# Kernel tuning notes

Measured on AMD Instinct MI355X. Metric: run time of the kernel, lower is better.

The kernel has to match this reference:

```python
import jax, jax.numpy as jnp
import numpy as np
from jax import lax

T, Nn, K, IN, H1, H2, G, P, HEADS = 64, 2048, 32, 256, 128, 128, 256, 60, 3


def setup_inputs() -> dict:
    key = jax.random.key(0)
    ks = jax.random.split(key, 20)
    s = 0.05  # weight scale to keep activations sane
    return {
        'h': jax.random.normal(ks[0], (T, Nn, IN), jnp.float32),
        'neigh': jax.random.randint(ks[1], (Nn, K), 0, Nn),
        'Npop': jnp.ones((1,), jnp.float32) * 1e6,
        'I': jax.random.uniform(ks[2], (T,), jnp.float32) * 1e4,
        'R': jax.random.uniform(ks[3], (T,), jnp.float32) * 1e4,
        'S': jax.random.uniform(ks[4], (T,), jnp.float32) * 9e5,
        'It': jax.random.uniform(ks[5], (T,), jnp.float32),
        'Rt': jax.random.uniform(ks[6], (T,), jnp.float32),
        'fc1': jax.random.normal(ks[7], (HEADS, IN, H1), jnp.float32) * s,
        'fc2': jax.random.normal(ks[8], (HEADS * H1, H2), jnp.float32) * s,
        'gru_Wih': jax.random.normal(ks[9], (3 * G, H2), jnp.float32) * s,
        'gru_Whh': jax.random.normal(ks[10], (3 * G, G), jnp.float32) * s,
        'gru_bih': jax.random.normal(ks[11], (3 * G,), jnp.float32) * s,
        'gru_bhh': jax.random.normal(ks[12], (3 * G,), jnp.float32) * s,
        'res1_W': jax.random.normal(ks[13], (2 * P, G + 2), jnp.float32) * s,
        'res1_b': jax.random.normal(ks[14], (2 * P,), jnp.float32) * s,
        'res2_W': jax.random.normal(ks[15], (2, G + 2), jnp.float32) * s,
        'res2_b': jax.random.normal(ks[16], (2,), jnp.float32) * s,
        'hx0': jax.random.normal(ks[17], (G,), jnp.float32),
    }


def _input_attention(iz, neigh):
    # cosine^4 edge scores, unnormalized weighted sum of neighbor feats
    src = iz[neigh]                                  # [N,K,d]
    dot = jnp.einsum('nkd,nd->nk', src, iz)
    nsrc = jnp.sqrt(jnp.einsum('nkd,nkd->nk', src, src))
    ndst = jnp.sqrt(jnp.sum(iz * iz, axis=-1))[:, None]
    e = (dot / nsrc / ndst) ** 4                     # [N,K]
    return jnp.einsum('nk,nkd->nd', e, src)


def _gat_head(x, W, neigh):
    # dot-product edge attention + per-node softmax + weighted reduce
    z = x @ W                                        # [N,H]
    src = z[neigh]                                   # [N,K,H]
    e = jnp.einsum('nkd,nd->nk', src, z)             # [N,K]
    a = jax.nn.softmax(e, axis=1)
    return jnp.einsum('nk,nkd->nd', a, src)


def _gru_cell(x, hx, Wih, Whh, bih, bhh):
    gi = Wih @ x + bih                               # [3G]
    gh = Whh @ hx + bhh
    ir, iz, inn = jnp.split(gi, 3)
    hr, hz, hn = jnp.split(gh, 3)
    r = jax.nn.sigmoid(ir + hr)
    zg = jax.nn.sigmoid(iz + hz)
    n = jnp.tanh(inn + r * hn)
    return (1.0 - zg) * n + zg * hx


def reference(h, neigh, Npop, I, R, S, It, Rt, fc1, fc2, gru_Wih, gru_Whh,
              gru_bih, gru_bhh, res1_W, res1_b, res2_W, res2_b, hx0):
    Np = Npop[0]

    def step(hx, xs):
        h_t, I_t, R_t, S_t, It_t, Rt_t = xs
        ih = _input_attention(h_t, neigh)                       # [N,in]
        heads = jax.vmap(lambda W: _gat_head(ih, W, neigh))(fc1)  # [3,N,H1]
        c = jax.nn.relu(jnp.transpose(heads, (1, 0, 2)).reshape(Nn, HEADS * H1))
        c = _gat_head(c, fc2, neigh)                            # [N,H2]
        pooled = jnp.max(jax.nn.relu(c), axis=0)                # [H2]
        hx = _gru_cell(pooled, hx, gru_Wih, gru_Whh, gru_bih, gru_bhh)
        nhx = jnp.concatenate([hx, It_t[None], Rt_t[None]])     # [G+2]
        pred = res1_W @ nhx + res1_b                            # [2P]
        ab = res2_W @ nhx + res2_b
        a_s = jax.nn.sigmoid(ab[0])
        b_s = jax.nn.sigmoid(ab[1])
        new_I = pred[0::2]
        new_R = pred[1::2]

        def sir(st, _):
            lI, lR, lS = st
            dI = a_s * lI * (lS / Np) - b_s * lI
            dR = b_s * lI
            nI = lI + lax.stop_gradient(dI)
            nR = lR + lax.stop_gradient(dR)
            nS = Np - nI - nR
            return (nI, nR, nS), (dI, dR)

        _, (pI, pR) = lax.scan(sir, (I_t, R_t, S_t), None, length=P)
        return hx, (new_I, new_R, pI, pR)

    _, (new_I, new_R, phy_I, phy_R) = lax.scan(step, hx0, (h, I, R, S, It, Rt))
    return (new_I, new_R, phy_I.reshape(-1), phy_R.reshape(-1))
```

## Files before the change

### kernel.cpp

```cpp
#include <hip/hip_runtime.h>
#include <hip/hip_bf16.h>
#include <math.h>

#define T_STEPS 64
#define NN      2048
#define KN      32
#define IND     256
#define H1D     128
#define C1D     384
#define H2D     128
#define GD      256
#define PD      60
#define GRU_NB  8

typedef __attribute__((ext_vector_type(8))) short bf16x8v;
typedef __attribute__((ext_vector_type(4))) float f32x4v;

#define BITREV5_INIT {0,16,8,24,4,20,12,28,2,18,10,26,6,22,14,30, \
                      1,17,9,25,5,21,13,29,3,19,11,27,7,23,15,31}

__device__ __forceinline__ float bcast_lane(float v, int lane_imm) {
    return __uint_as_float(__builtin_amdgcn_readlane(__float_as_uint(v), lane_imm));
}

__device__ __forceinline__ void bf16_split(float v, __hip_bfloat16* hi, __hip_bfloat16* lo) {
    __hip_bfloat16 h = __float2bfloat16(v);
    *hi = h;
    *lo = __float2bfloat16(v - __bfloat162float(h));
}

__device__ __forceinline__ float xpose_reduce16(float part[16], int lane) {
#pragma unroll
    for (int i = 0; i < 8; ++i) {
        float send = (lane & 2) ? part[i] : part[i + 8];
        float keep = (lane & 2) ? part[i + 8] : part[i];
        part[i] = keep + __shfl_xor(send, 2);
    }
#pragma unroll
    for (int i = 0; i < 4; ++i) {
        float send = (lane & 4) ? part[i] : part[i + 4];
        float keep = (lane & 4) ? part[i + 4] : part[i];
        part[i] = keep + __shfl_xor(send, 4);
    }
#pragma unroll
    for (int i = 0; i < 2; ++i) {
        float send = (lane & 8) ? part[i] : part[i + 2];
        float keep = (lane & 8) ? part[i + 2] : part[i];
        part[i] = keep + __shfl_xor(send, 8);
    }
    {
        float send = (lane & 16) ? part[0] : part[1];
        float keep = (lane & 16) ? part[1] : part[0];
        part[0] = keep + __shfl_xor(send, 16);
    }
    return part[0] + __shfl_xor(part[0], 32);
}

__global__ __launch_bounds__(256) void norms_kernel(const float* __restrict__ h,
                                                    float* __restrict__ norms,
                                                    int t_base) {
    int gw   = (int)((blockIdx.x * blockDim.x + threadIdx.x) >> 6);
    int lane = threadIdx.x & 63;
    int n    = gw & (NN - 1);
    int tloc = gw >> 11;
    const float4* row = (const float4*)(h + ((size_t)(t_base + tloc) * NN + n) * IND);
    float4 v = row[lane];
    float s = v.x * v.x + v.y * v.y + v.z * v.z + v.w * v.w;
#pragma unroll
    for (int off = 32; off > 0; off >>= 1) s += __shfl_xor(s, off);
    if (lane == 0) norms[(size_t)tloc * NN + n] = sqrtf(s);
}

__global__ __launch_bounds__(256, 4) void input_attn_kernel(const float* __restrict__ h,
                                                            const int* __restrict__ neigh,
                                                            const float* __restrict__ norms,
                                                            __hip_bfloat16* __restrict__ ihHi,
                                                            __hip_bfloat16* __restrict__ ihLo,
                                                            int t_base) {
    const int BR[32] = BITREV5_INIT;
    __shared__ float hd_s[2][2][32];
    int wave    = threadIdx.x >> 6;
    int nodeloc = wave >> 1;
    int half    = wave & 1;
    int lane    = threadIdx.x & 63;
    int gw   = (int)((blockIdx.x << 1) | nodeloc);
    int n    = gw & (NN - 1);
    int tloc = gw >> 11;
    const float* hT  = h + (size_t)(t_base + tloc) * NN * IND;
    const float* nrm = norms + (size_t)tloc * NN;

    const float* dst = hT + (size_t)n * IND + half * 128;
    float d0 = dst[lane], d1 = dst[lane + 64];

    int   jreg = neigh[n * KN + (lane & 31)];
    float nj   = nrm[jreg];
    float ndst = nrm[n];

    float r0[32], r1[32], comb[16];
#pragma unroll
    for (int i = 0; i < 16; ++i) {
        int sja = __builtin_amdgcn_readlane(jreg, BR[i]);
        int sjb = __builtin_amdgcn_readlane(jreg, BR[i + 16]);
        const float* sa = hT + (size_t)sja * IND + half * 128;
        const float* sb = hT + (size_t)sjb * IND + half * 128;
        r0[i]      = sa[lane]; r1[i]      = sa[lane + 64];
        r0[i + 16] = sb[lane]; r1[i + 16] = sb[lane + 64];
        float pa = r0[i] * d0 + r1[i] * d1;
        float pb = r0[i + 16] * d0 + r1[i + 16] * d1;
        float send = (lane & 1) ? pa : pb;
        float keep = (lane & 1) ? pb : pa;
        comb[i] = keep + __shfl_xor(send, 1);
    }
#pragma unroll
    for (int i = 0; i < 32; ++i) asm volatile("" : "+v"(r0[i]), "+v"(r1[i]));
    float hdot = xpose_reduce16(comb, lane);
    if (lane < 32) hd_s[nodeloc][half][lane] = hdot;
    __syncthreads();
    float dot = hdot + hd_s[nodeloc][half ^ 1][lane & 31];

    float r  = dot / (nj * ndst);
    float r2 = r * r;
    float e  = r2 * r2;

    float a0 = 0.f, a1 = 0.f;
#pragma unroll
    for (int i = 0; i < 32; ++i) {
        float ek = bcast_lane(e, BR[i]);
        a0 += ek * r0[i];
        a1 += ek * r1[i];
    }
    size_t base = (size_t)gw * IND + half * 128;
    __hip_bfloat16 hi, lo;
    bf16_split(a0, &hi, &lo);
    ihHi[base + lane] = hi;       ihLo[base + lane] = lo;
    bf16_split(a1, &hi, &lo);
    ihHi[base + lane + 64] = hi;  ihLo[base + lane + 64] = lo;
}

__global__ __launch_bounds__(256) void gemm_bf16x3(const __hip_bfloat16* __restrict__ Ahi,
                                                   const __hip_bfloat16* __restrict__ Alo,
                                                   const __hip_bfloat16* __restrict__ BThi,
                                                   const __hip_bfloat16* __restrict__ BTlo,
                                                   float* __restrict__ C,
                                                   int M, int N, int K) {
    int lane = threadIdx.x & 63;
    int w    = threadIdx.x >> 6;
    int m0   = blockIdx.y * 64 + w * 16;
    int n0   = blockIdx.x * 64;
    int r    = lane & 15;
    int g    = lane >> 4;

    const __hip_bfloat16* arow_hi = Ahi + (size_t)(m0 + r) * K + g * 8;
    const __hip_bfloat16* arow_lo = Alo + (size_t)(m0 + r) * K + g * 8;

    f32x4v acc[4] = {};
    for (int k0 = 0; k0 < K; k0 += 32) {
        bf16x8v ah = *(const bf16x8v*)(arow_hi + k0);
        bf16x8v al = *(const bf16x8v*)(arow_lo + k0);
#pragma unroll
        for (int nt = 0; nt < 4; ++nt) {
            size_t boff = (size_t)(n0 + nt * 16 + r) * K + g * 8 + k0;
            bf16x8v bh = *(const bf16x8v*)(BThi + boff);
            bf16x8v bl = *(const bf16x8v*)(BTlo + boff);
            acc[nt] = __builtin_amdgcn_mfma_f32_16x16x32_bf16(ah, bh, acc[nt], 0, 0, 0);
            acc[nt] = __builtin_amdgcn_mfma_f32_16x16x32_bf16(ah, bl, acc[nt], 0, 0, 0);
            acc[nt] = __builtin_amdgcn_mfma_f32_16x16x32_bf16(al, bh, acc[nt], 0, 0, 0);
        }
    }
#pragma unroll
    for (int nt = 0; nt < 4; ++nt)
#pragma unroll
        for (int q = 0; q < 4; ++q)
            C[(size_t)(m0 + g * 4 + q) * N + n0 + nt * 16 + r] = acc[nt][q];
}

__global__ __launch_bounds__(192, 4) void gat_heads_kernel(const float* __restrict__ z1,
                                                           const int* __restrict__ neigh,
                                                           __hip_bfloat16* __restrict__ cHi,
                                                           __hip_bfloat16* __restrict__ cLo) {
    const int BR[32] = BITREV5_INIT;
    int n    = blockIdx.x & (NN - 1);
    const float* ztbl = z1 + (size_t)(blockIdx.x >> 11) * NN * C1D;
    int head = threadIdx.x >> 6;
    int lane = threadIdx.x & 63;

    const float* dst = ztbl + (size_t)n * C1D + head * H1D;
    float d0 = dst[lane], d1 = dst[lane + 64];
    int jreg = neigh[n * KN + (lane & 31)];

    float r0[32], r1[32], comb[16];
#pragma unroll
    for (int i = 0; i < 16; ++i) {
        int sja = __builtin_amdgcn_readlane(jreg, BR[i]);
        int sjb = __builtin_amdgcn_readlane(jreg, BR[i + 16]);
        const float* sa = ztbl + (size_t)sja * C1D + head * H1D;
        const float* sb = ztbl + (size_t)sjb * C1D + head * H1D;
        r0[i]      = sa[lane]; r1[i]      = sa[lane + 64];
        r0[i + 16] = sb[lane]; r1[i + 16] = sb[lane + 64];
        float pa = r0[i] * d0 + r1[i] * d1;
        float pb = r0[i + 16] * d0 + r1[i + 16] * d1;
        float send = (lane & 1) ? pa : pb;
        float keep = (lane & 1) ? pb : pa;
        comb[i] = keep + __shfl_xor(send, 1);
    }
#pragma unroll
    for (int i = 0; i < 32; ++i) asm volatile("" : "+v"(r0[i]), "+v"(r1[i]));
    float dot = xpose_reduce16(comb, lane);

    float m = dot;
#pragma unroll
    for (int off = 16; off > 0; off >>= 1) m = fmaxf(m, __shfl_xor(m, off));
    float p = __expf(dot - m);
    float s = p;
#pragma unroll
    for (int off = 16; off > 0; off >>= 1) s += __shfl_xor(s, off);
    p /= s;

    float a0 = 0.f, a1 = 0.f;
#pragma unroll
    for (int i = 0; i < 32; ++i) {
        float pk = bcast_lane(p, BR[i]);
        a0 += pk * r0[i];
        a1 += pk * r1[i];
    }
    size_t base = (size_t)blockIdx.x * C1D + (size_t)head * H1D;
    __hip_bfloat16 hi, lo;
    bf16_split(fmaxf(a0, 0.f), &hi, &lo);
    cHi[base + lane] = hi;       cLo[base + lane] = lo;
    bf16_split(fmaxf(a1, 0.f), &hi, &lo);
    cHi[base + lane + 64] = hi;  cLo[base + lane + 64] = lo;
}

__global__ __launch_bounds__(256, 4) void gat_final_kernel(const float* __restrict__ z2,
                                                           const int* __restrict__ neigh,
                                                           float* __restrict__ c2) {
    const int BR[32] = BITREV5_INIT;
    int gw   = (int)((blockIdx.x << 2) | (threadIdx.x >> 6));
    int n    = gw & (NN - 1);
    const float* ztbl = z2 + (size_t)(gw >> 11) * NN * H2D;
    int lane = threadIdx.x & 63;

    const float* dst = ztbl + (size_t)n * H2D;
    float d0 = dst[lane], d1 = dst[lane + 64];
    int jreg = neigh[n * KN + (lane & 31)];

    float r0[32], r1[32], comb[16];
#pragma unroll
    for (int i = 0; i < 16; ++i) {
        int sja = __builtin_amdgcn_readlane(jreg, BR[i]);
        int sjb = __builtin_amdgcn_readlane(jreg, BR[i + 16]);
        const float* sa = ztbl + (size_t)sja * H2D;
        const float* sb = ztbl + (size_t)sjb * H2D;
        r0[i]      = sa[lane]; r1[i]      = sa[lane + 64];
        r0[i + 16] = sb[lane]; r1[i + 16] = sb[lane + 64];
        float pa = r0[i] * d0 + r1[i] * d1;
        float pb = r0[i + 16] * d0 + r1[i + 16] * d1;
        float send = (lane & 1) ? pa : pb;
        float keep = (lane & 1) ? pb : pa;
        comb[i] = keep + __shfl_xor(send, 1);
    }
#pragma unroll
    for (int i = 0; i < 32; ++i) asm volatile("" : "+v"(r0[i]), "+v"(r1[i]));
    float dot = xpose_reduce16(comb, lane);

    float m = dot;
#pragma unroll
    for (int off = 16; off > 0; off >>= 1) m = fmaxf(m, __shfl_xor(m, off));
    float p = __expf(dot - m);
    float s = p;
#pragma unroll
    for (int off = 16; off > 0; off >>= 1) s += __shfl_xor(s, off);
    p /= s;

    float a0 = 0.f, a1 = 0.f;
#pragma unroll
    for (int i = 0; i < 32; ++i) {
        float pk = bcast_lane(p, BR[i]);
        a0 += pk * r0[i];
        a1 += pk * r1[i];
    }
    c2[(size_t)gw * H2D + lane]      = fmaxf(a0, 0.f);
    c2[(size_t)gw * H2D + lane + 64] = fmaxf(a1, 0.f);
}

__global__ __launch_bounds__(128) void pool_part_kernel(const float* __restrict__ c2,
                                                        float* __restrict__ ppart) {
    int j = threadIdx.x;
    int tloc  = blockIdx.x >> 4;
    int slice = blockIdx.x & 15;
    const float* base = c2 + ((size_t)tloc * NN + slice * 128) * H2D;
    float mx = 0.f;
    for (int q = 0; q < 128; ++q) mx = fmaxf(mx, base[(size_t)q * H2D + j]);
    ppart[(size_t)blockIdx.x * H2D + j] = mx;
}
__global__ __launch_bounds__(128) void pool_reduce_kernel(const float* __restrict__ ppart,
                                                          float* __restrict__ pooled,
                                                          int t_base) {
    int j = threadIdx.x;
    const float* base = ppart + (size_t)blockIdx.x * 16 * H2D;
    float mx = 0.f;
#pragma unroll
    for (int q = 0; q < 16; ++q) mx = fmaxf(mx, base[(size_t)q * H2D + j]);
    pooled[(t_base + blockIdx.x) * H2D + j] = mx;
}

__global__ void prep_kernel(const float* __restrict__ fc1, const float* __restrict__ fc2,
                            __hip_bfloat16* __restrict__ W1Thi, __hip_bfloat16* __restrict__ W1Tlo,
                            __hip_bfloat16* __restrict__ f2Thi, __hip_bfloat16* __restrict__ f2Tlo,
                            unsigned int* __restrict__ cnt) {
    int i = blockIdx.x * 256 + threadIdx.x;
    if (i < 384 * 256) {
        int cf = i / 256, d = i % 256;
        int hd = cf >> 7, j = cf & 127;
        float v = fc1[(size_t)hd * 256 * 128 + (size_t)d * 128 + j];
        __hip_bfloat16 hi, lo;
        bf16_split(v, &hi, &lo);
        W1Thi[i] = hi; W1Tlo[i] = lo;
    }
    if (i < 128 * 384) {
        int n = i / 384, k = i % 384;
        float v = fc2[(size_t)k * 128 + n];
        __hip_bfloat16 hi, lo;
        bf16_split(v, &hi, &lo);
        f2Thi[i] = hi; f2Tlo[i] = lo;
    }
    if (i < T_STEPS) cnt[i] = 0u;
}

__global__ __launch_bounds__(256) void gi_all_kernel(const float* __restrict__ Wih,
                                                     const float* __restrict__ bih,
                                                     const float* __restrict__ pooled,
                                                     float* __restrict__ gi_all) {
    __shared__ float p_s[H2D];
    int t  = blockIdx.x / 3;
    int ob = (blockIdx.x % 3) * 256;
    if (threadIdx.x < H2D) p_s[threadIdx.x] = pooled[t * H2D + threadIdx.x];
    __syncthreads();
    int o = ob + threadIdx.x;
    float acc = bih[o];
    const float* wr = Wih + (size_t)o * H2D;
#pragma unroll 4
    for (int d = 0; d < H2D; ++d) acc += wr[d] * p_s[d];
    gi_all[t * 768 + o] = acc;
}

__global__ __launch_bounds__(768) void gru_reg_kernel(const float* __restrict__ Whh,
                                                      const float* __restrict__ bhh,
                                                      const float* __restrict__ gi_all,
                                                      const float* __restrict__ hx0,
                                                      float* hx_all,
                                                      unsigned int* cnt) {
    __shared__ float4 hx_pad[72];
    __shared__ __align__(16) float hx_lin[GD];
    __shared__ float gh_s[96];
    int b   = blockIdx.x;
    int tid = threadIdx.x;
    int row_local = tid >> 3;
    int sub       = tid & 7;
    int chunk     = row_local >> 5;
    int r_in      = row_local & 31;
    int grow      = chunk * GD + b * 32 + r_in;

    float4 wreg[8];
    const float4* wrow = (const float4*)(Whh + (size_t)grow * GD + sub * 32);
#pragma unroll
    for (int i = 0; i < 8; ++i) wreg[i] = wrow[i];
    float bias = (sub == 0) ? bhh[grow] : 0.f;

    for (int t = 0; t < T_STEPS; ++t) {
        if (t > 0) {
            if (tid == 0) {
                while (__hip_atomic_load(&cnt[t - 1], __ATOMIC_ACQUIRE,
                                         __HIP_MEMORY_SCOPE_AGENT) < GRU_NB)
                    __builtin_amdgcn_s_sleep(1);
            }
            __syncthreads();
        }
        const float* hsrc = (t == 0) ? hx0 : (hx_all + (size_t)(t - 1) * GD);
        if (tid < 64) {
            float4 v;
            v.x = __hip_atomic_load(hsrc + tid * 4 + 0, __ATOMIC_RELAXED, __HIP_MEMORY_SCOPE_AGENT);
            v.y = __hip_atomic_load(hsrc + tid * 4 + 1, __ATOMIC_RELAXED, __HIP_MEMORY_SCOPE_AGENT);
            v.z = __hip_atomic_load(hsrc + tid * 4 + 2, __ATOMIC_RELAXED, __HIP_MEMORY_SCOPE_AGENT);
            v.w = __hip_atomic_load(hsrc + tid * 4 + 3, __ATOMIC_RELAXED, __HIP_MEMORY_SCOPE_AGENT);
            hx_pad[(tid >> 3) * 9 + (tid & 7)] = v;
            ((float4*)hx_lin)[tid] = v;
        }
        __syncthreads();

        float acc = 0.f;
#pragma unroll
        for (int i = 0; i < 8; ++i) {
            float4 hv = hx_pad[sub * 9 + i];
            float4 wv = wreg[i];
            acc += wv.x * hv.x + wv.y * hv.y + wv.z * hv.z + wv.w * hv.w;
        }
        acc += __shfl_xor(acc, 1);
        acc += __shfl_xor(acc, 2);
        acc += __shfl_xor(acc, 4);
        if (sub == 0) gh_s[row_local] = acc + bias;
        __syncthreads();

        if (tid < 32) {
            int u = b * 32 + tid;
            float gi_r = gi_all[t * 768 + u];
            float gi_z = gi_all[t * 768 + 256 + u];
            float gi_n = gi_all[t * 768 + 512 + u];
            float r  = 1.f / (1.f + expf(-(gi_r + gh_s[tid])));
            float zg = 1.f / (1.f + expf(-(gi_z + gh_s[32 + tid])));
            float nn = tanhf(gi_n + r * gh_s[64 + tid]);
            float hnew = (1.f - zg) * nn + zg * hx_lin[u];
            __hip_atomic_store(&hx_all[(size_t)t * GD + u], hnew,
                               __ATOMIC_RELAXED, __HIP_MEMORY_SCOPE_AGENT);
        }
        __syncthreads();
        if (tid == 0)
            __hip_atomic_fetch_add(&cnt[t], 1u, __ATOMIC_RELEASE,
                                   __HIP_MEMORY_SCOPE_AGENT);
    }
}

__global__ __launch_bounds__(128) void res_sir_kernel(const float* __restrict__ hx_all,
                                                      const float* __restrict__ It,
                                                      const float* __restrict__ Rt,
                                                      const float* __restrict__ r1W,
                                                      const float* __restrict__ r1b,
                                                      const float* __restrict__ r2W,
                                                      const float* __restrict__ r2b,
                                                      const float* __restrict__ I,
                                                      const float* __restrict__ R,
                                                      const float* __restrict__ S,
                                                      const float* __restrict__ Npop,
                                                      float* __restrict__ out) {
    __shared__ float nhx[258];
    __shared__ float ab_s[2];
    int t = blockIdx.x, tid = threadIdx.x;
    for (int i = tid; i < GD; i += 128) nhx[i] = hx_all[t * GD + i];
    if (tid == 0) { nhx[256] = It[t]; nhx[257] = Rt[t]; }
    __syncthreads();
    if (tid < 120) {
        float acc = r1b[tid];
        const float* wr = r1W + tid * 258;
        for (int d = 0; d < 258; ++d) acc += wr[d] * nhx[d];
        int idx = t * 60 + (tid >> 1);
        if (tid & 1) out[3840 + idx] = acc;
        else         out[idx] = acc;
    }
    if (tid == 120 || tid == 121) {
        int q = tid - 120;
        float acc = r2b[q];
        const float* wr = r2W + q * 258;
        for (int d = 0; d < 258; ++d) acc += wr[d] * nhx[d];
        ab_s[q] = acc;
    }
    __syncthreads();
    if (tid == 0) {
        float a_s = 1.f / (1.f + expf(-ab_s[0]));
        float b_s = 1.f / (1.f + expf(-ab_s[1]));
        float Np = Npop[0];
        float lI = I[t], lR = R[t], lS = S[t];
        for (int p = 0; p < PD; ++p) {
            float dI = a_s * lI * (lS / Np) - b_s * lI;
            float dR = b_s * lI;
            lI += dI;
            lR += dR;
            lS = Np - lI - lR;
            out[7680  + t * 60 + p] = dI;
            out[11520 + t * 60 + p] = dR;
        }
    }
}

extern "C" void kernel_launch(void* const* d_in, const int* in_sizes, int n_in,
                              void* d_out, int out_size, void* d_ws, size_t ws_size,
                              hipStream_t stream) {
    const float* h    = (const float*)d_in[0];
    const int*   ng   = (const int*)  d_in[1];
    const float* Npop = (const float*)d_in[2];
    const float* I_   = (const float*)d_in[3];
    const float* R_   = (const float*)d_in[4];
    const float* S_   = (const float*)d_in[5];
    const float* It   = (const float*)d_in[6];
    const float* Rt   = (const float*)d_in[7];
    const float* fc1  = (const float*)d_in[8];
    const float* fc2  = (const float*)d_in[9];
    const float* gWih = (const float*)d_in[10];
    const float* gWhh = (const float*)d_in[11];
    const float* gbih = (const float*)d_in[12];
    const float* gbhh = (const float*)d_in[13];
    const float* r1W  = (const float*)d_in[14];
    const float* r1b  = (const float*)d_in[15];
    const float* r2W  = (const float*)d_in[16];
    const float* r2b  = (const float*)d_in[17];
    const float* hx0  = (const float*)d_in[18];
    float* out = (float*)d_out;

    char* w = (char*)d_ws;
    float* pooled = (float*)w; w += (size_t)T_STEPS * H2D * 4;
    float* hx_all = (float*)w; w += (size_t)T_STEPS * GD * 4;
    float* gi_all = (float*)w; w += (size_t)T_STEPS * 768 * 4;
    float* ppart  = (float*)w; w += (size_t)T_STEPS * 16 * H2D * 4;
    __hip_bfloat16* W1Thi = (__hip_bfloat16*)w; w += (size_t)384 * 256 * 2;
    __hip_bfloat16* W1Tlo = (__hip_bfloat16*)w; w += (size_t)384 * 256 * 2;
    __hip_bfloat16* f2Thi = (__hip_bfloat16*)w; w += (size_t)128 * 384 * 2;
    __hip_bfloat16* f2Tlo = (__hip_bfloat16*)w; w += (size_t)128 * 384 * 2;
    unsigned int* cnt = (unsigned int*)w; w += 256;
    size_t fixed = (size_t)(w - (char*)d_ws);

    const size_t perTc = 8192 + 2097152 + 3145728 + 3145728;
    int Tc = 16;
    while (Tc > 1) {
        if (fixed + (size_t)Tc * perTc <= ws_size) break;
        Tc >>= 1;
    }
    float* norms = (float*)w;             w += (size_t)Tc * NN * 4;
    char*  pairA = w;                     w += (size_t)Tc * NN * 256 * 2 * 2;
    float* z1    = (float*)w;             w += (size_t)Tc * NN * C1D * 4;
    __hip_bfloat16* cHi = (__hip_bfloat16*)w; w += (size_t)Tc * NN * C1D * 2;
    __hip_bfloat16* cLo = (__hip_bfloat16*)w;

    __hip_bfloat16* ihHi = (__hip_bfloat16*)pairA;
    __hip_bfloat16* ihLo = ihHi + (size_t)Tc * NN * 256;
    float* z2 = (float*)pairA;
    float* c2 = z2 + (size_t)Tc * NN * H2D;

    prep_kernel<<<(384 * 256 + 255) / 256, 256, 0, stream>>>(fc1, fc2, W1Thi, W1Tlo,
                                                             f2Thi, f2Tlo, cnt);

    for (int t0 = 0; t0 < T_STEPS; t0 += Tc) {
        int M = Tc * NN;
        norms_kernel      <<<Tc * NN / 4, 256, 0, stream>>>(h, norms, t0);
        input_attn_kernel <<<Tc * NN / 2, 256, 0, stream>>>(h, ng, norms, ihHi, ihLo, t0);
        gemm_bf16x3<<<dim3(384 / 64, M / 64), 256, 0, stream>>>(ihHi, ihLo, W1Thi, W1Tlo,
                                                                z1, M, 384, 256);
        gat_heads_kernel  <<<Tc * NN, 192, 0, stream>>>(z1, ng, cHi, cLo);
        gemm_bf16x3<<<dim3(128 / 64, M / 64), 256, 0, stream>>>(cHi, cLo, f2Thi, f2Tlo,
                                                                z2, M, 128, 384);
        gat_final_kernel  <<<Tc * NN / 4, 256, 0, stream>>>(z2, ng, c2);
        pool_part_kernel  <<<Tc * 16, 128, 0, stream>>>(c2, ppart);
        pool_reduce_kernel<<<Tc, 128, 0, stream>>>(ppart, pooled, t0);
    }

    gi_all_kernel<<<T_STEPS * 3, 256, 0, stream>>>(gWih, gbih, pooled, gi_all);
    gru_reg_kernel<<<GRU_NB, 768, 0, stream>>>(gWhh, gbhh, gi_all, hx0, hx_all, cnt);
    res_sir_kernel<<<T_STEPS, 128, 0, stream>>>(hx_all, It, Rt, r1W, r1b, r2W, r2b,
                                                I_, R_, S_, Npop, out);
}
```

Measured before the change: 1.695 ms.

## Split neighbor gathers across two waves per node to halve register footprint

The three gather-attention kernels (input attention, GAT heads, final GAT) now split the 32 neighbors of each node across two waves of 16 each, so each wave keeps only 16 gathered rows in registers instead of 32. Partial dot products and partial weighted sums are exchanged through shared memory, and the softmax max and sum are combined across the two halves. Launch bounds rise to 6 waves per SIMD to exploit the lower register pressure for more latency hiding on the random gathers. The cost is twice as many waves doing the same memory traffic, extra LDS exchanges and block-wide barriers, and half the waves idling during the final write.

Result: slower. 1.777 ms (+4.9%).

```diff
diff --git a/kernel.cpp b/kernel.cpp
--- a/kernel.cpp
+++ b/kernel.cpp
@@ -16,8 +16,7 @@
 typedef __attribute__((ext_vector_type(8))) short bf16x8v;
 typedef __attribute__((ext_vector_type(4))) float f32x4v;
 
-#define BITREV5_INIT {0,16,8,24,4,20,12,28,2,18,10,26,6,22,14,30, \
-                      1,17,9,25,5,21,13,29,3,19,11,27,7,23,15,31}
+#define BITREV4_INIT {0,8,4,12,2,10,6,14,1,9,5,13,3,11,7,15}
 
 __device__ __forceinline__ float bcast_lane(float v, int lane_imm) {
     return __uint_as_float(__builtin_amdgcn_readlane(__float_as_uint(v), lane_imm));
@@ -29,31 +28,26 @@
     *lo = __float2bfloat16(v - __bfloat162float(h));
 }
 
-__device__ __forceinline__ float xpose_reduce16(float part[16], int lane) {
-#pragma unroll
-    for (int i = 0; i < 8; ++i) {
-        float send = (lane & 2) ? part[i] : part[i + 8];
-        float keep = (lane & 2) ? part[i + 8] : part[i];
+__device__ __forceinline__ float xpose_reduce8(float part[8], int lane) {
+#pragma unroll
+    for (int i = 0; i < 4; ++i) {
+        float send = (lane & 2) ? part[i] : part[i + 4];
+        float keep = (lane & 2) ? part[i + 4] : part[i];
         part[i] = keep + __shfl_xor(send, 2);
     }
 #pragma unroll
-    for (int i = 0; i < 4; ++i) {
-        float send = (lane & 4) ? part[i] : part[i + 4];
-        float keep = (lane & 4) ? part[i + 4] : part[i];
+    for (int i = 0; i < 2; ++i) {
+        float send = (lane & 4) ? part[i] : part[i + 2];
+        float keep = (lane & 4) ? part[i + 2] : part[i];
         part[i] = keep + __shfl_xor(send, 4);
     }
-#pragma unroll
-    for (int i = 0; i < 2; ++i) {
-        float send = (lane & 8) ? part[i] : part[i + 2];
-        float keep = (lane & 8) ? part[i + 2] : part[i];
-        part[i] = keep + __shfl_xor(send, 8);
-    }
     {
-        float send = (lane & 16) ? part[0] : part[1];
-        float keep = (lane & 16) ? part[1] : part[0];
-        part[0] = keep + __shfl_xor(send, 16);
-    }
-    return part[0] + __shfl_xor(part[0], 32);
+        float send = (lane & 8) ? part[0] : part[1];
+        float keep = (lane & 8) ? part[1] : part[0];
+        part[0] = keep + __shfl_xor(send, 8);
+    }
+    float r = part[0] + __shfl_xor(part[0], 16);
+    return r + __shfl_xor(r, 32);
 }
 
 __global__ __launch_bounds__(256) void norms_kernel(const float* __restrict__ h,
@@ -71,52 +65,53 @@
     if (lane == 0) norms[(size_t)tloc * NN + n] = sqrtf(s);
 }
 
-__global__ __launch_bounds__(256, 4) void input_attn_kernel(const float* __restrict__ h,
+__global__ __launch_bounds__(256, 6) void input_attn_kernel(const float* __restrict__ h,
                                                             const int* __restrict__ neigh,
                                                             const float* __restrict__ norms,
                                                             __hip_bfloat16* __restrict__ ihHi,
                                                             __hip_bfloat16* __restrict__ ihLo,
                                                             int t_base) {
-    const int BR[32] = BITREV5_INIT;
-    __shared__ float hd_s[2][2][32];
-    int wave    = threadIdx.x >> 6;
-    int nodeloc = wave >> 1;
-    int half    = wave & 1;
-    int lane    = threadIdx.x & 63;
-    int gw   = (int)((blockIdx.x << 1) | nodeloc);
+    const int BR[16] = BITREV4_INIT;
+    __shared__ float hd_s[2][2][16];
+    __shared__ float acc_s[2][128];
+    int wave = threadIdx.x >> 6;
+    int hd   = wave >> 1;
+    int hk   = wave & 1;
+    int lane = threadIdx.x & 63;
+    int gw   = blockIdx.x;
     int n    = gw & (NN - 1);
     int tloc = gw >> 11;
     const float* hT  = h + (size_t)(t_base + tloc) * NN * IND;
     const float* nrm = norms + (size_t)tloc * NN;
 
-    const float* dst = hT + (size_t)n * IND + half * 128;
+    const float* dst = hT + (size_t)n * IND + hd * 128;
     float d0 = dst[lane], d1 = dst[lane + 64];
 
-    int   jreg = neigh[n * KN + (lane & 31)];
+    int   jreg = neigh[n * KN + hk * 16 + (lane & 15)];
     float nj   = nrm[jreg];
     float ndst = nrm[n];
 
-    float r0[32], r1[32], comb[16];
-#pragma unroll
-    for (int i = 0; i < 16; ++i) {
+    float r0[16], r1[16], comb[8];
+#pragma unroll
+    for (int i = 0; i < 8; ++i) {
         int sja = __builtin_amdgcn_readlane(jreg, BR[i]);
-        int sjb = __builtin_amdgcn_readlane(jreg, BR[i + 16]);
-        const float* sa = hT + (size_t)sja * IND + half * 128;
-        const float* sb = hT + (size_t)sjb * IND + half * 128;
-        r0[i]      = sa[lane]; r1[i]      = sa[lane + 64];
-        r0[i + 16] = sb[lane]; r1[i + 16] = sb[lane + 64];
+        int sjb = __builtin_amdgcn_readlane(jreg, BR[i + 8]);
+        const float* sa = hT + (size_t)sja * IND + hd * 128;
+        const float* sb = hT + (size_t)sjb * IND + hd * 128;
+        r0[i]     = sa[lane]; r1[i]     = sa[lane + 64];
+        r0[i + 8] = sb[lane]; r1[i + 8] = sb[lane + 64];
         float pa = r0[i] * d0 + r1[i] * d1;
-        float pb = r0[i + 16] * d0 + r1[i + 16] * d1;
+        float pb = r0[i + 8] * d0 + r1[i + 8] * d1;
         float send = (lane & 1) ? pa : pb;
         float keep = (lane & 1) ? pb : pa;
         comb[i] = keep + __shfl_xor(send, 1);
     }
 #pragma unroll
-    for (int i = 0; i < 32; ++i) asm volatile("" : "+v"(r0[i]), "+v"(r1[i]));
-    float hdot = xpose_reduce16(comb, lane);
-    if (lane < 32) hd_s[nodeloc][half][lane] = hdot;
-    __syncthreads();
-    float dot = hdot + hd_s[nodeloc][half ^ 1][lane & 31];
+    for (int i = 0; i < 16; ++i) asm volatile("" : "+v"(r0[i]), "+v"(r1[i]));
+    float hdot = xpose_reduce8(comb, lane);
+    if (lane < 16) hd_s[hd][hk][lane] = hdot;
+    __syncthreads();
+    float dot = hdot + hd_s[hd ^ 1][hk][lane & 15];
 
     float r  = dot / (nj * ndst);
     float r2 = r * r;
@@ -124,17 +119,23 @@
 
     float a0 = 0.f, a1 = 0.f;
 #pragma unroll
-    for (int i = 0; i < 32; ++i) {
+    for (int i = 0; i < 16; ++i) {
         float ek = bcast_lane(e, BR[i]);
         a0 += ek * r0[i];
         a1 += ek * r1[i];
     }
-    size_t base = (size_t)gw * IND + half * 128;
-    __hip_bfloat16 hi, lo;
-    bf16_split(a0, &hi, &lo);
-    ihHi[base + lane] = hi;       ihLo[base + lane] = lo;
-    bf16_split(a1, &hi, &lo);
-    ihHi[base + lane + 64] = hi;  ihLo[base + lane + 64] = lo;
+    if (hk == 0) { acc_s[hd][lane] = a0; acc_s[hd][lane + 64] = a1; }
+    __syncthreads();
+    if (hk == 1) {
+        float t0 = a0 + acc_s[hd][lane];
+        float t1 = a1 + acc_s[hd][lane + 64];
+        size_t base = (size_t)gw * IND + hd * 128;
+        __hip_bfloat16 hi, lo;
+        bf16_split(t0, &hi, &lo);
+        ihHi[base + lane] = hi;       ihLo[base + lane] = lo;
+        bf16_split(t1, &hi, &lo);
+        ihHi[base + lane + 64] = hi;  ihLo[base + lane + 64] = lo;
+    }
 }
 
 __global__ __launch_bounds__(256) void gemm_bf16x3(const __hip_bfloat16* __restrict__ Ahi,
@@ -174,113 +175,142 @@
             C[(size_t)(m0 + g * 4 + q) * N + n0 + nt * 16 + r] = acc[nt][q];
 }
 
-__global__ __launch_bounds__(192, 4) void gat_heads_kernel(const float* __restrict__ z1,
+__global__ __launch_bounds__(384, 6) void gat_heads_kernel(const float* __restrict__ z1,
                                                            const int* __restrict__ neigh,
                                                            __hip_bfloat16* __restrict__ cHi,
                                                            __hip_bfloat16* __restrict__ cLo) {
-    const int BR[32] = BITREV5_INIT;
+    const int BR[16] = BITREV4_INIT;
+    __shared__ float dots_s[3][2][16];
+    __shared__ float accs[3][128];
     int n    = blockIdx.x & (NN - 1);
     const float* ztbl = z1 + (size_t)(blockIdx.x >> 11) * NN * C1D;
-    int head = threadIdx.x >> 6;
+    int wave = threadIdx.x >> 6;
+    int head = wave >> 1;
+    int kh   = wave & 1;
     int lane = threadIdx.x & 63;
 
     const float* dst = ztbl + (size_t)n * C1D + head * H1D;
     float d0 = dst[lane], d1 = dst[lane + 64];
-    int jreg = neigh[n * KN + (lane & 31)];
-
-    float r0[32], r1[32], comb[16];
-#pragma unroll
-    for (int i = 0; i < 16; ++i) {
+    int jreg = neigh[n * KN + kh * 16 + (lane & 15)];
+
+    float r0[16], r1[16], comb[8];
+#pragma unroll
+    for (int i = 0; i < 8; ++i) {
         int sja = __builtin_amdgcn_readlane(jreg, BR[i]);
-        int sjb = __builtin_amdgcn_readlane(jreg, BR[i + 16]);
+        int sjb = __builtin_amdgcn_readlane(jreg, BR[i + 8]);
         const float* sa = ztbl + (size_t)sja * C1D + head * H1D;
         const float* sb = ztbl + (size_t)sjb * C1D + head * H1D;
-        r0[i]      = sa[lane]; r1[i]      = sa[lane + 64];
-        r0[i + 16] = sb[lane]; r1[i + 16] = sb[lane + 64];
+        r0[i]     = sa[lane]; r1[i]     = sa[lane + 64];
+        r0[i + 8] = sb[lane]; r1[i + 8] = sb[lane + 64];
         float pa = r0[i] * d0 + r1[i] * d1;
-        float pb = r0[i + 16] * d0 + r1[i + 16] * d1;
+        float pb = r0[i + 8] * d0 + r1[i + 8] * d1;
         float send = (lane & 1) ? pa : pb;
         float keep = (lane & 1) ? pb : pa;
         comb[i] = keep + __shfl_xor(send, 1);
     }
 #pragma unroll
-    for (int i = 0; i < 32; ++i) asm volatile("" : "+v"(r0[i]), "+v"(r1[i]));
-    float dot = xpose_reduce16(comb, lane);
-
-    float m = dot;
-#pragma unroll
-    for (int off = 16; off > 0; off >>= 1) m = fmaxf(m, __shfl_xor(m, off));
-    float p = __expf(dot - m);
-    float s = p;
-#pragma unroll
-    for (int off = 16; off > 0; off >>= 1) s += __shfl_xor(s, off);
-    p /= s;
+    for (int i = 0; i < 16; ++i) asm volatile("" : "+v"(r0[i]), "+v"(r1[i]));
+    float dot = xpose_reduce8(comb, lane);
+
+    if (lane < 16) dots_s[head][kh][lane] = dot;
+    __syncthreads();
+    float dOth = dots_s[head][kh ^ 1][lane & 15];
+
+    float mx = fmaxf(dot, dOth);
+#pragma unroll
+    for (int off = 8; off > 0; off >>= 1) mx = fmaxf(mx, __shfl_xor(mx, off));
+    float eMine = __expf(dot - mx);
+    float eOth  = __expf(dOth - mx);
+    float ss = eMine + eOth;
+#pragma unroll
+    for (int off = 8; off > 0; off >>= 1) ss += __shfl_xor(ss, off);
+    float p = eMine / ss;
 
     float a0 = 0.f, a1 = 0.f;
 #pragma unroll
-    for (int i = 0; i < 32; ++i) {
+    for (int i = 0; i < 16; ++i) {
         float pk = bcast_lane(p, BR[i]);
         a0 += pk * r0[i];
         a1 += pk * r1[i];
     }
-    size_t base = (size_t)blockIdx.x * C1D + (size_t)head * H1D;
-    __hip_bfloat16 hi, lo;
-    bf16_split(fmaxf(a0, 0.f), &hi, &lo);
-    cHi[base + lane] = hi;       cLo[base + lane] = lo;
-    bf16_split(fmaxf(a1, 0.f), &hi, &lo);
-    cHi[base + lane + 64] = hi;  cLo[base + lane + 64] = lo;
-}
-
-__global__ __launch_bounds__(256, 4) void gat_final_kernel(const float* __restrict__ z2,
+    if (kh == 0) { accs[head][lane] = a0; accs[head][lane + 64] = a1; }
+    __syncthreads();
+    if (kh == 1) {
+        float t0 = fmaxf(a0 + accs[head][lane], 0.f);
+        float t1 = fmaxf(a1 + accs[head][lane + 64], 0.f);
+        size_t base = (size_t)blockIdx.x * C1D + (size_t)head * H1D;
+        __hip_bfloat16 hi, lo;
+        bf16_split(t0, &hi, &lo);
+        cHi[base + lane] = hi;       cLo[base + lane] = lo;
+        bf16_split(t1, &hi, &lo);
+        cHi[base + lane + 64] = hi;  cLo[base + lane + 64] = lo;
+    }
+}
+
+__global__ __launch_bounds__(256, 6) void gat_final_kernel(const float* __restrict__ z2,
                                                            const int* __restrict__ neigh,
                                                            float* __restrict__ c2) {
-    const int BR[32] = BITREV5_INIT;
-    int gw   = (int)((blockIdx.x << 2) | (threadIdx.x >> 6));
+    const int BR[16] = BITREV4_INIT;
+    __shared__ float dots_s[2][2][16];
+    __shared__ float accs[2][128];
+    int wave    = threadIdx.x >> 6;
+    int nodeloc = wave >> 1;
+    int kh      = wave & 1;
+    int lane    = threadIdx.x & 63;
+    int gw   = (int)((blockIdx.x << 1) | nodeloc);
     int n    = gw & (NN - 1);
     const float* ztbl = z2 + (size_t)(gw >> 11) * NN * H2D;
-    int lane = threadIdx.x & 63;
 
     const float* dst = ztbl + (size_t)n * H2D;
     float d0 = dst[lane], d1 = dst[lane + 64];
-    int jreg = neigh[n * KN + (lane & 31)];
-
-    float r0[32], r1[32], comb[16];
-#pragma unroll
-    for (int i = 0; i < 16; ++i) {
+    int jreg = neigh[n * KN + kh * 16 + (lane & 15)];
+
+    float r0[16], r1[16], comb[8];
+#pragma unroll
+    for (int i = 0; i < 8; ++i) {
         int sja = __builtin_amdgcn_readlane(jreg, BR[i]);
-        int sjb = __builtin_amdgcn_readlane(jreg, BR[i + 16]);
+        int sjb = __builtin_amdgcn_readlane(jreg, BR[i + 8]);
         const float* sa = ztbl + (size_t)sja * H2D;
         const float* sb = ztbl + (size_t)sjb * H2D;
-        r0[i]      = sa[lane]; r1[i]      = sa[lane + 64];
-        r0[i + 16] = sb[lane]; r1[i + 16] = sb[lane + 64];
+        r0[i]     = sa[lane]; r1[i]     = sa[lane + 64];
+        r0[i + 8] = sb[lane]; r1[i + 8] = sb[lane + 64];
         float pa = r0[i] * d0 + r1[i] * d1;
-        float pb = r0[i + 16] * d0 + r1[i + 16] * d1;
+        float pb = r0[i + 8] * d0 + r1[i + 8] * d1;
         float send = (lane & 1) ? pa : pb;
         float keep = (lane & 1) ? pb : pa;
         comb[i] = keep + __shfl_xor(send, 1);
     }
 #pragma unroll
-    for (int i = 0; i < 32; ++i) asm volatile("" : "+v"(r0[i]), "+v"(r1[i]));
-    float dot = xpose_reduce16(comb, lane);
-
-    float m = dot;
-#pragma unroll
-    for (int off = 16; off > 0; off >>= 1) m = fmaxf(m, __shfl_xor(m, off));
-    float p = __expf(dot - m);
-    float s = p;
-#pragma unroll
-    for (int off = 16; off > 0; off >>= 1) s += __shfl_xor(s, off);
-    p /= s;
+    for (int i = 0; i < 16; ++i) asm volatile("" : "+v"(r0[i]), "+v"(r1[i]));
+    float dot = xpose_reduce8(comb, lane);
+
+    if (lane < 16) dots_s[nodeloc][kh][lane] = dot;
+    __syncthreads();
+    float dOth = dots_s[nodeloc][kh ^ 1][lane & 15];
+
+    float mx = fmaxf(dot, dOth);
+#pragma unroll
+    for (int off = 8; off > 0; off >>= 1) mx = fmaxf(mx, __shfl_xor(mx, off));
+    float eMine = __expf(dot - mx);
+    float eOth  = __expf(dOth - mx);
+    float ss = eMine + eOth;
+#pragma unroll
+    for (int off = 8; off > 0; off >>= 1) ss += __shfl_xor(ss, off);
+    float p = eMine / ss;
 
     float a0 = 0.f, a1 = 0.f;
 #pragma unroll
-    for (int i = 0; i < 32; ++i) {
+    for (int i = 0; i < 16; ++i) {
         float pk = bcast_lane(p, BR[i]);
         a0 += pk * r0[i];
         a1 += pk * r1[i];
     }
-    c2[(size_t)gw * H2D + lane]      = fmaxf(a0, 0.f);
-    c2[(size_t)gw * H2D + lane + 64] = fmaxf(a1, 0.f);
+    if (kh == 0) { accs[nodeloc][lane] = a0; accs[nodeloc][lane + 64] = a1; }
+    __syncthreads();
+    if (kh == 1) {
+        c2[(size_t)gw * H2D + lane]      = fmaxf(a0 + accs[nodeloc][lane], 0.f);
+        c2[(size_t)gw * H2D + lane + 64] = fmaxf(a1 + accs[nodeloc][lane + 64], 0.f);
+    }
 }
 
 __global__ __launch_bounds__(128) void pool_part_kernel(const float* __restrict__ c2,
@@ -530,13 +560,13 @@
     for (int t0 = 0; t0 < T_STEPS; t0 += Tc) {
         int M = Tc * NN;
         norms_kernel      <<<Tc * NN / 4, 256, 0, stream>>>(h, norms, t0);
-        input_attn_kernel <<<Tc * NN / 2, 256, 0, stream>>>(h, ng, norms, ihHi, ihLo, t0);
+        input_attn_kernel <<<Tc * NN,     256, 0, stream>>>(h, ng, norms, ihHi, ihLo, t0);
         gemm_bf16x3<<<dim3(384 / 64, M / 64), 256, 0, stream>>>(ihHi, ihLo, W1Thi, W1Tlo,
                                                                 z1, M, 384, 256);
-        gat_heads_kernel  <<<Tc * NN, 192, 0, stream>>>(z1, ng, cHi, cLo);
+        gat_heads_kernel  <<<Tc * NN, 384, 0, stream>>>(z1, ng, cHi, cLo);
         gemm_bf16x3<<<dim3(128 / 64, M / 64), 256, 0, stream>>>(cHi, cLo, f2Thi, f2Tlo,
                                                                 z2, M, 128, 384);
-        gat_final_kernel  <<<Tc * NN / 4, 256, 0, stream>>>(z2, ng, c2);
+        gat_final_kernel  <<<Tc * NN / 2, 256, 0, stream>>>(z2, ng, c2);
         pool_part_kernel  <<<Tc * 16, 128, 0, stream>>>(c2, ppart);
         pool_reduce_kernel<<<Tc, 128, 0, stream>>>(ppart, pooled, t0);
     }
```

## Stage GEMM tiles in LDS and fuse max-pool partials into GAT final kernel

Applied to the files above, without the earlier changes.

The bf16x3 GEMM now loads A and B tiles cooperatively into shared memory each k-step instead of having every wave re-read B from global memory, which cuts redundant global traffic. The final GAT kernel no longer writes the full c2 activation. It reduces its four nodes' ReLU outputs to a per-block max and writes that to ppart, which removes the pool_part kernel and the c2 round trip. In exchange, pool_reduce now loops over 512 partials per timestep with few blocks, which may serialize, and the GEMM adds two barriers per k-step.

Measured after the change: 1.566 ms. 1.08x faster.

```diff
diff --git a/kernel.cpp b/kernel.cpp
--- a/kernel.cpp
+++ b/kernel.cpp
@@ -143,25 +143,34 @@
                                                    const __hip_bfloat16* __restrict__ BTlo,
                                                    float* __restrict__ C,
                                                    int M, int N, int K) {
-    int lane = threadIdx.x & 63;
-    int w    = threadIdx.x >> 6;
-    int m0   = blockIdx.y * 64 + w * 16;
+    __shared__ short Ah[64][40], Al[64][40], Bh[64][40], Bl[64][40];
+    int tid  = threadIdx.x;
+    int lane = tid & 63;
+    int w    = tid >> 6;
+    int mb   = blockIdx.y * 64;
     int n0   = blockIdx.x * 64;
     int r    = lane & 15;
     int g    = lane >> 4;
-
-    const __hip_bfloat16* arow_hi = Ahi + (size_t)(m0 + r) * K + g * 8;
-    const __hip_bfloat16* arow_lo = Alo + (size_t)(m0 + r) * K + g * 8;
+    int lrow = tid >> 2;
+    int lseg = tid & 3;
+
+    const size_t aoff = (size_t)(mb + lrow) * K + lseg * 8;
+    const size_t boff = (size_t)(n0 + lrow) * K + lseg * 8;
 
     f32x4v acc[4] = {};
     for (int k0 = 0; k0 < K; k0 += 32) {
-        bf16x8v ah = *(const bf16x8v*)(arow_hi + k0);
-        bf16x8v al = *(const bf16x8v*)(arow_lo + k0);
+        __syncthreads();
+        *(bf16x8v*)&Ah[lrow][lseg * 8] = *(const bf16x8v*)(Ahi + aoff + k0);
+        *(bf16x8v*)&Al[lrow][lseg * 8] = *(const bf16x8v*)(Alo + aoff + k0);
+        *(bf16x8v*)&Bh[lrow][lseg * 8] = *(const bf16x8v*)(BThi + boff + k0);
+        *(bf16x8v*)&Bl[lrow][lseg * 8] = *(const bf16x8v*)(BTlo + boff + k0);
+        __syncthreads();
+        bf16x8v ah = *(const bf16x8v*)&Ah[w * 16 + r][g * 8];
+        bf16x8v al = *(const bf16x8v*)&Al[w * 16 + r][g * 8];
 #pragma unroll
         for (int nt = 0; nt < 4; ++nt) {
-            size_t boff = (size_t)(n0 + nt * 16 + r) * K + g * 8 + k0;
-            bf16x8v bh = *(const bf16x8v*)(BThi + boff);
-            bf16x8v bl = *(const bf16x8v*)(BTlo + boff);
+            bf16x8v bh = *(const bf16x8v*)&Bh[nt * 16 + r][g * 8];
+            bf16x8v bl = *(const bf16x8v*)&Bl[nt * 16 + r][g * 8];
             acc[nt] = __builtin_amdgcn_mfma_f32_16x16x32_bf16(ah, bh, acc[nt], 0, 0, 0);
             acc[nt] = __builtin_amdgcn_mfma_f32_16x16x32_bf16(ah, bl, acc[nt], 0, 0, 0);
             acc[nt] = __builtin_amdgcn_mfma_f32_16x16x32_bf16(al, bh, acc[nt], 0, 0, 0);
@@ -171,7 +180,7 @@
     for (int nt = 0; nt < 4; ++nt)
 #pragma unroll
         for (int q = 0; q < 4; ++q)
-            C[(size_t)(m0 + g * 4 + q) * N + n0 + nt * 16 + r] = acc[nt][q];
+            C[(size_t)(mb + w * 16 + g * 4 + q) * N + n0 + nt * 16 + r] = acc[nt][q];
 }
 
 __global__ __launch_bounds__(192, 4) void gat_heads_kernel(const float* __restrict__ z1,
@@ -233,9 +242,11 @@
 
 __global__ __launch_bounds__(256, 4) void gat_final_kernel(const float* __restrict__ z2,
                                                            const int* __restrict__ neigh,
-                                                           float* __restrict__ c2) {
+                                                           float* __restrict__ ppart) {
     const int BR[32] = BITREV5_INIT;
-    int gw   = (int)((blockIdx.x << 2) | (threadIdx.x >> 6));
+    __shared__ float red_s[4][128];
+    int wave = threadIdx.x >> 6;
+    int gw   = (int)((blockIdx.x << 2) | wave);
     int n    = gw & (NN - 1);
     const float* ztbl = z2 + (size_t)(gw >> 11) * NN * H2D;
     int lane = threadIdx.x & 63;
@@ -279,28 +290,25 @@
         a0 += pk * r0[i];
         a1 += pk * r1[i];
     }
-    c2[(size_t)gw * H2D + lane]      = fmaxf(a0, 0.f);
-    c2[(size_t)gw * H2D + lane + 64] = fmaxf(a1, 0.f);
-}
-
-__global__ __launch_bounds__(128) void pool_part_kernel(const float* __restrict__ c2,
-                                                        float* __restrict__ ppart) {
-    int j = threadIdx.x;
-    int tloc  = blockIdx.x >> 4;
-    int slice = blockIdx.x & 15;
-    const float* base = c2 + ((size_t)tloc * NN + slice * 128) * H2D;
-    float mx = 0.f;
-    for (int q = 0; q < 128; ++q) mx = fmaxf(mx, base[(size_t)q * H2D + j]);
-    ppart[(size_t)blockIdx.x * H2D + j] = mx;
-}
+    red_s[wave][lane]      = fmaxf(a0, 0.f);
+    red_s[wave][lane + 64] = fmaxf(a1, 0.f);
+    __syncthreads();
+    int tid = threadIdx.x;
+    if (tid < 128) {
+        float mx = fmaxf(fmaxf(red_s[0][tid], red_s[1][tid]),
+                         fmaxf(red_s[2][tid], red_s[3][tid]));
+        ppart[(size_t)blockIdx.x * H2D + tid] = mx;
+    }
+}
+
 __global__ __launch_bounds__(128) void pool_reduce_kernel(const float* __restrict__ ppart,
                                                           float* __restrict__ pooled,
                                                           int t_base) {
     int j = threadIdx.x;
-    const float* base = ppart + (size_t)blockIdx.x * 16 * H2D;
+    const float* base = ppart + (size_t)blockIdx.x * 512 * H2D;
     float mx = 0.f;
-#pragma unroll
-    for (int q = 0; q < 16; ++q) mx = fmaxf(mx, base[(size_t)q * H2D + j]);
+#pragma unroll 8
+    for (int q = 0; q < 512; ++q) mx = fmaxf(mx, base[(size_t)q * H2D + j]);
     pooled[(t_base + blockIdx.x) * H2D + j] = mx;
 }
 
@@ -499,7 +507,7 @@
     float* pooled = (float*)w; w += (size_t)T_STEPS * H2D * 4;
     float* hx_all = (float*)w; w += (size_t)T_STEPS * GD * 4;
     float* gi_all = (float*)w; w += (size_t)T_STEPS * 768 * 4;
-    float* ppart  = (float*)w; w += (size_t)T_STEPS * 16 * H2D * 4;
+    float* ppart  = (float*)w; w += (size_t)16 * 512 * H2D * 4;
     __hip_bfloat16* W1Thi = (__hip_bfloat16*)w; w += (size_t)384 * 256 * 2;
     __hip_bfloat16* W1Tlo = (__hip_bfloat16*)w; w += (size_t)384 * 256 * 2;
     __hip_bfloat16* f2Thi = (__hip_bfloat16*)w; w += (size_t)128 * 384 * 2;
@@ -522,7 +530,6 @@
     __hip_bfloat16* ihHi = (__hip_bfloat16*)pairA;
     __hip_bfloat16* ihLo = ihHi + (size_t)Tc * NN * 256;
     float* z2 = (float*)pairA;
-    float* c2 = z2 + (size_t)Tc * NN * H2D;
 
     prep_kernel<<<(384 * 256 + 255) / 256, 256, 0, stream>>>(fc1, fc2, W1Thi, W1Tlo,
                                                              f2Thi, f2Tlo, cnt);
@@ -536,8 +543,7 @@
         gat_heads_kernel  <<<Tc * NN, 192, 0, stream>>>(z1, ng, cHi, cLo);
         gemm_bf16x3<<<dim3(128 / 64, M / 64), 256, 0, stream>>>(cHi, cLo, f2Thi, f2Tlo,
                                                                 z2, M, 128, 384);
-        gat_final_kernel  <<<Tc * NN / 4, 256, 0, stream>>>(z2, ng, c2);
-        pool_part_kernel  <<<Tc * 16, 128, 0, stream>>>(c2, ppart);
+        gat_final_kernel  <<<Tc * NN / 4, 256, 0, stream>>>(z2, ng, ppart);
         pool_reduce_kernel<<<Tc, 128, 0, stream>>>(ppart, pooled, t0);
     }
 
```
